# Kernel optimization log

Hardware: AMD Instinct MI355X
Metric: run time of the kernel (lower is better)

The kernel has to match this reference:

```python
import jax, jax.numpy as jnp
import numpy as np

D_MODEL = 1024
D_INNER = 2048
D_STATE = 16
DT_RANK = 64  # ceil(1024/16)
N_LAYERS = 4
SEQ = 4096


def setup_inputs() -> dict:
    key = jax.random.key(0)
    ks = list(jax.random.split(key, 8))
    L, d, di, n, r = N_LAYERS, D_MODEL, D_INNER, D_STATE, DT_RANK
    def rn(k, shape, scale):
        return jax.random.normal(k, shape, dtype=jnp.float32) * scale
    A_init = jnp.tile(jnp.log(jnp.arange(1, n + 1, dtype=jnp.float32))[None, None, :], (L, di, 1))
    return {
        'x': jax.random.normal(ks[0], (SEQ, d), dtype=jnp.float32),
        'pos_enc': jax.random.normal(ks[1], (SEQ, d), dtype=jnp.float32),
        'ln_g': jnp.ones((d,), jnp.float32),
        'ln_b': jnp.zeros((d,), jnp.float32),
        'innorm_g': jnp.ones((L, d), jnp.float32),
        'innorm_b': jnp.zeros((L, d), jnp.float32),
        'in_proj_w': rn(ks[2], (L, 2 * di, d), 0.02),
        'in_proj_b': jnp.zeros((L, 2 * di), jnp.float32),
        'conv_w': rn(ks[3], (L, di, 1, 3), 0.1),
        'conv_b': jnp.zeros((L, di), jnp.float32),
        'deltaBC_w': rn(ks[4], (L, r + 2 * n, di), 0.02),
        'dt_proj_w': rn(ks[5], (L, di, r), 0.02),
        'dt_proj_b': jnp.zeros((L, di), jnp.float32),
        'A_log': A_init,
        'Dp': jnp.ones((L, di), jnp.float32),
        'outnorm_g': jnp.ones((L, di), jnp.float32),
        'outnorm_b': jnp.zeros((L, di), jnp.float32),
        'out_proj_w': rn(ks[6], (L, d, di), 0.02),
        'out_proj_b': jnp.zeros((L, d), jnp.float32),
    }


def _ln(x, g, b, eps):
    mu = jnp.mean(x, axis=-1, keepdims=True)
    var = jnp.mean((x - mu) ** 2, axis=-1, keepdims=True)
    return (x - mu) * jax.lax.rsqrt(var + eps) * g + b


def _selective_scan(u, delta, A, B, C, D):
    # u, delta: [b,l,d]; A: [d,n]; B, C: [b,l,n]; D: [d]
    b, l, d = u.shape
    n = A.shape[1]
    def step(h, inputs):
        d_t, B_t, u_t, C_t = inputs          # [b,d],[b,n],[b,d],[b,n]
        dA = jnp.exp(d_t[:, :, None] * A)    # [b,d,n]
        dBu = (d_t * u_t)[:, :, None] * B_t[:, None, :]
        h = dA * h + dBu
        y = jnp.einsum('bdn,bn->bd', h, C_t)
        return h, y
    h0 = jnp.zeros((b, d, n), u.dtype)
    xs = (jnp.swapaxes(delta, 0, 1), jnp.swapaxes(B, 0, 1),
          jnp.swapaxes(u, 0, 1), jnp.swapaxes(C, 0, 1))
    _, ys = jax.lax.scan(step, h0, xs)       # ys: [l,b,d]
    return jnp.swapaxes(ys, 0, 1) + u * D


def _block(x, innorm_g, innorm_b, in_proj_w, in_proj_b, conv_w, conv_b,
           deltaBC_w, dt_proj_w, dt_proj_b, A_log, Dp, outnorm_g, outnorm_b,
           out_proj_w, out_proj_b):
    skip = x
    h = _ln(x, innorm_g, innorm_b, 1e-5)
    xz = h @ in_proj_w.T + in_proj_b
    x1, z1 = jnp.split(xz, 2, axis=-1)       # [b,s,di] each
    # depthwise conv1d, k=3, pad=1
    xc = jnp.swapaxes(x1, 1, 2)              # [b,di,s]
    xc = jax.lax.conv_general_dilated(xc, conv_w, (1,), [(1, 1)],
                                      feature_group_count=xc.shape[1],
                                      dimension_numbers=('NCH', 'OIH', 'NCH'))
    xc = xc + conv_b[None, :, None]
    u = jnp.swapaxes(xc, 1, 2)               # [b,s,di]
    # SSM
    A = -jnp.exp(A_log)
    dbc = u @ deltaBC_w.T                    # [b,s,r+2n]
    delta, B, C = jnp.split(dbc, [DT_RANK, DT_RANK + D_STATE], axis=-1)
    delta = jax.nn.softplus(delta @ dt_proj_w.T + dt_proj_b)
    y = _selective_scan(u, delta, A, B, C, Dp)
    y = _ln(y, outnorm_g, outnorm_b, 1e-5)
    out = y * jax.nn.silu(z1)
    return out @ out_proj_w.T + out_proj_b + skip


def _forward(x, pos_enc, ln_g, ln_b, innorm_g, innorm_b, in_proj_w, in_proj_b,
             conv_w, conv_b, deltaBC_w, dt_proj_w, dt_proj_b, A_log, Dp,
             outnorm_g, outnorm_b, out_proj_w, out_proj_b):
    enc = _ln(x + pos_enc, ln_g, ln_b, 1e-6)[None]  # [1,s,d]
    for i in range(N_LAYERS):
        enc = _block(enc, innorm_g[i], innorm_b[i], in_proj_w[i], in_proj_b[i],
                     conv_w[i], conv_b[i], deltaBC_w[i], dt_proj_w[i],
                     dt_proj_b[i], A_log[i], Dp[i], outnorm_g[i], outnorm_b[i],
                     out_proj_w[i], out_proj_b[i])
    return enc[0]


def reference(x, pos_enc, ln_g, ln_b, innorm_g, innorm_b, in_proj_w, in_proj_b,
              conv_w, conv_b, deltaBC_w, dt_proj_w, dt_proj_b, A_log, Dp,
              outnorm_g, outnorm_b, out_proj_w, out_proj_b):
    return _forward(x, pos_enc, ln_g, ln_b, innorm_g, innorm_b, in_proj_w,
                    in_proj_b, conv_w, conv_b, deltaBC_w, dt_proj_w, dt_proj_b,
                    A_log, Dp, outnorm_g, outnorm_b, out_proj_w, out_proj_b)
```

## Files before the change

### kernel.cpp

```cpp
#include <hip/hip_runtime.h>
#include <hip/hip_bf16.h>
#include <stdint.h>


#define SEQ     4096
#define DMODEL  1024
#define DINNER  2048
#define NSTATE  16
#define DTRANK  64
#define NLAYERS 4
#define LC      64
#define NC      64

typedef __attribute__((ext_vector_type(8))) short short8v;
typedef __attribute__((ext_vector_type(4))) float f32x4;
typedef __hip_bfloat16 bf16;

__device__ __forceinline__ float b2f(unsigned short x) {
    unsigned int u = ((unsigned int)x) << 16;
    return __builtin_bit_cast(float, u);
}

__device__ __forceinline__ void gld16(const void* gsrc, void* ldst) {
    __builtin_amdgcn_global_load_lds(
        (const __attribute__((address_space(1))) void*)gsrc,
        (__attribute__((address_space(3))) void*)ldst, 16, 0, 0);
}

__device__ __forceinline__ float block_sum(float v, float* red, int nwaves) {
    #pragma unroll
    for (int o = 32; o > 0; o >>= 1) v += __shfl_down(v, o, 64);
    int lane = threadIdx.x & 63, w = threadIdx.x >> 6;
    __syncthreads();
    if (lane == 0) red[w] = v;
    __syncthreads();
    float s = red[0];
    for (int i = 1; i < nwaves; i++) s += red[i];
    return s;
}

template<int WIDTH, typename OutT>
__global__ void ln_kernel(const float* __restrict__ X, const float* __restrict__ X2,
                          const float* __restrict__ g, const float* __restrict__ bta,
                          OutT* __restrict__ out, float eps) {
    constexpr int E = WIDTH / 256;
    __shared__ float red[4];
    int s = blockIdx.x, tid = threadIdx.x;
    size_t base = (size_t)s * WIDTH;
    float v[E]; float sum = 0.f;
    #pragma unroll
    for (int i = 0; i < E; i++) {
        int c = tid + i * 256;
        float t = X[base + c];
        if (X2) t += X2[base + c];
        v[i] = t; sum += t;
    }
    float mu = block_sum(sum, red, 4) * (1.f / WIDTH);
    float sq = 0.f;
    #pragma unroll
    for (int i = 0; i < E; i++) { float d = v[i] - mu; sq += d * d; }
    float var = block_sum(sq, red, 4) * (1.f / WIDTH);
    float rstd = rsqrtf(var + eps);
    #pragma unroll
    for (int i = 0; i < E; i++) {
        int c = tid + i * 256;
        float r = (v[i] - mu) * rstd * g[c] + bta[c];
        out[base + c] = (OutT)r;
    }
}

__global__ void outnorm_silu_kernel(const float* __restrict__ y, const bf16* __restrict__ xz,
                                    const float* __restrict__ g, const float* __restrict__ bta,
                                    bf16* __restrict__ p_bf, float eps) {
    constexpr int WIDTH = DINNER, E = WIDTH / 256;
    __shared__ float red[4];
    int s = blockIdx.x, tid = threadIdx.x;
    size_t base = (size_t)s * WIDTH;
    const unsigned short* xzu = (const unsigned short*)xz;
    float v[E]; float sum = 0.f;
    #pragma unroll
    for (int i = 0; i < E; i++) { int c = tid + i * 256; v[i] = y[base + c]; sum += v[i]; }
    float mu = block_sum(sum, red, 4) * (1.f / WIDTH);
    float sq = 0.f;
    #pragma unroll
    for (int i = 0; i < E; i++) { float d = v[i] - mu; sq += d * d; }
    float var = block_sum(sq, red, 4) * (1.f / WIDTH);
    float rstd = rsqrtf(var + eps);
    #pragma unroll
    for (int i = 0; i < E; i++) {
        int c = tid + i * 256;
        float ln = (v[i] - mu) * rstd * g[c] + bta[c];
        float z = b2f(xzu[(size_t)s * (2 * DINNER) + DINNER + c]);
        float sig = 1.f / (1.f + __expf(-z));
        p_bf[base + c] = __float2bfloat16(ln * (z * sig));
    }
}

__global__ void conv_kernel(const bf16* __restrict__ xz, const float* __restrict__ cw,
                            const float* __restrict__ cb, bf16* __restrict__ u_bf) {
    int t = blockIdx.x * 256 + threadIdx.x;
    int s = t >> 9, c = (t & 511) * 4;
    size_t row = (size_t)s * (2 * DINNER);
    const unsigned short* xp = (const unsigned short*)xz;
    ushort4 z4 = {0, 0, 0, 0};
    ushort4 v0 = *(const ushort4*)(xp + row + c);
    ushort4 vm = (s > 0)       ? *(const ushort4*)(xp + row - 2 * DINNER + c) : z4;
    ushort4 vp = (s < SEQ - 1) ? *(const ushort4*)(xp + row + 2 * DINNER + c) : z4;
    unsigned short o[4];
    float x0[4] = {b2f(v0.x), b2f(v0.y), b2f(v0.z), b2f(v0.w)};
    float xm[4] = {b2f(vm.x), b2f(vm.y), b2f(vm.z), b2f(vm.w)};
    float xp4[4] = {b2f(vp.x), b2f(vp.y), b2f(vp.z), b2f(vp.w)};
    #pragma unroll
    for (int i = 0; i < 4; i++) {
        int ch = c + i;
        float u = cw[ch * 3 + 0] * xm[i] + cw[ch * 3 + 1] * x0[i]
                + cw[ch * 3 + 2] * xp4[i] + cb[ch];
        o[i] = __builtin_bit_cast(unsigned short, __float2bfloat16(u));
    }
    *(ushort4*)((unsigned short*)u_bf + (size_t)s * DINNER + c) = {o[0], o[1], o[2], o[3]};
}

#define CN0 (2 * DINNER * DMODEL)
#define CN1 (DMODEL * DINNER)
#define CN2 (96 * DINNER)
#define CN3 (DINNER * DTRANK)
__global__ void cvt_all_kernel(const float* __restrict__ w0, const float* __restrict__ w1,
                               const float* __restrict__ w2, const float* __restrict__ w3,
                               bf16* __restrict__ o0, bf16* __restrict__ o1,
                               bf16* __restrict__ o2, bf16* __restrict__ o3) {
    size_t i = (size_t)(blockIdx.x * 256 + threadIdx.x) * 4;
    const float* src; bf16* dst;
    if (i < CN0)                   { src = w0; dst = o0; }
    else if (i < CN0 + CN1)        { src = w1; dst = o1; i -= CN0; }
    else if (i < CN0 + CN1 + CN2)  { src = w2; dst = o2; i -= CN0 + CN1; }
    else                           { src = w3; dst = o3; i -= CN0 + CN1 + CN2; }
    float4 v = *(const float4*)(src + i);
    __hip_bfloat162 t0, t1;
    t0.x = __float2bfloat16(v.x); t0.y = __float2bfloat16(v.y);
    t1.x = __float2bfloat16(v.z); t1.y = __float2bfloat16(v.w);
    __hip_bfloat162* o = (__hip_bfloat162*)(dst + i);
    o[0] = t0; o[1] = t1;
}

template<int MODE>
__global__ __launch_bounds__(256, 2)
void mfma_gemm(const bf16* __restrict__ A, int lda,
               const bf16* __restrict__ W, int ldw,
               const float* __restrict__ bias,
               float* __restrict__ C, int ldc,
               const float* __restrict__ res,
               bf16* __restrict__ Cbf,
               int M, int N, int K) {
    __shared__ __attribute__((aligned(16))) short sA[128][32];
    __shared__ __attribute__((aligned(16))) short sB[128][32];
    int tid = threadIdx.x;
    int lane = tid & 63, w = tid >> 6;
    int wm = w >> 1, wn = w & 1;
    int m0 = blockIdx.x * 128, n0 = blockIdx.y * 128;
    int r16 = lane & 15, quad = lane >> 4;
    int ldrow = (lane >> 2);
    int c8 = (lane & 3) * 8;

    if (MODE == 1) {
        int kz = blockIdx.z;
        A += (size_t)kz * K;
        W += (size_t)kz * K;
        C += (size_t)kz * M * 96;
    }

    f32x4 acc[4][4] = {};

    for (int k0 = 0; k0 < K; k0 += 32) {
        __syncthreads();
        #pragma unroll
        for (int j = 0; j < 2; j++) {
            int row = j * 64 + w * 16 + ldrow;
            gld16(A + (size_t)(m0 + row) * lda + k0 + c8,
                  (char*)&sA[0][0] + j * 4096 + w * 1024);
            int nr = n0 + row; if (nr > N - 1) nr = N - 1;
            gld16(W + (size_t)nr * ldw + k0 + c8,
                  (char*)&sB[0][0] + j * 4096 + w * 1024);
        }
        __syncthreads();
        short8v aF[4], bF[4];
        #pragma unroll
        for (int mi = 0; mi < 4; mi++)
            aF[mi] = *(const short8v*)&sA[wm * 64 + mi * 16 + r16][quad * 8];
        #pragma unroll
        for (int ni = 0; ni < 4; ni++)
            bF[ni] = *(const short8v*)&sB[wn * 64 + ni * 16 + r16][quad * 8];
        #pragma unroll
        for (int mi = 0; mi < 4; mi++)
            #pragma unroll
            for (int ni = 0; ni < 4; ni++)
                acc[mi][ni] = __builtin_amdgcn_mfma_f32_16x16x32_bf16(
                    aF[mi], bF[ni], acc[mi][ni], 0, 0, 0);
    }

    #pragma unroll
    for (int mi = 0; mi < 4; mi++) {
        #pragma unroll
        for (int ni = 0; ni < 4; ni++) {
            f32x4 a = acc[mi][ni];
            int col = n0 + wn * 64 + ni * 16 + r16;
            int rbase = m0 + wm * 64 + mi * 16 + quad * 4;
            #pragma unroll
            for (int r = 0; r < 4; r++) {
                int row = rbase + r;
                float v = a[r];
                if (MODE == 0 || MODE == 2 || MODE == 3) v += bias[col];
                if (MODE == 2) v = (v > 20.f) ? v : log1pf(__expf(v));
                if (MODE == 3) v += res[(size_t)row * ldc + col];
                if (MODE == 1) {
                    if (col < 96) C[(size_t)row * 96 + col] = v;
                } else if (MODE == 0) {
                    Cbf[(size_t)row * ldc + col] = __float2bfloat16(v);
                } else {
                    C[(size_t)row * ldc + col] = v;
                }
            }
        }
    }
}

__global__ void reduce_dbc_kernel(const float* __restrict__ p, float* __restrict__ dbc,
                                  bf16* __restrict__ dbc_bf) {
    int i = blockIdx.x * 256 + threadIdx.x;
    const int SP = SEQ * 96;
    float v = p[i] + p[i + SP] + p[i + 2 * SP] + p[i + 3 * SP];
    dbc[i] = v;
    int row = i / 96, c = i - row * 96;
    if (c < DTRANK) dbc_bf[(size_t)row * DTRANK + c] = __float2bfloat16(v);
}

__device__ __forceinline__ bool a_is_neg_integers(const float* a) {
    bool fast = true;
    #pragma unroll
    for (int n = 0; n < NSTATE; n++)
        fast = fast && (__builtin_fabsf(a[n] + (float)(n + 1)) < 1e-3f * (n + 1));
    return fast;
}

__global__ void scan1_kernel(const float* __restrict__ delta, const bf16* __restrict__ u,
                             const float* __restrict__ dbc, const float* __restrict__ A_log,
                             float* __restrict__ h_end, float* __restrict__ dsum) {
    __shared__ __attribute__((aligned(16))) float sB[LC][NSTATE];
    int k = blockIdx.x, d = blockIdx.y * 256 + threadIdx.x;
    int s0 = k * LC, tid = threadIdx.x;
    #pragma unroll
    for (int i = 0; i < 4; i++) {
        int idx = tid + i * 256;
        int r = idx >> 4, n = idx & 15;
        sB[r][n] = dbc[(size_t)(s0 + r) * 96 + DTRANK + n];
    }
    float a[NSTATE];
    #pragma unroll
    for (int n = 0; n < NSTATE; n++) a[n] = -__expf(A_log[(size_t)d * NSTATE + n]);
    bool fast = a_is_neg_integers(a);
    __syncthreads();
    const unsigned short* uu16 = (const unsigned short*)u;
    float h[NSTATE] = {}; float ds = 0.f;
    if (fast) {
        #pragma unroll 2
        for (int r = 0; r < LC; r++) {
            float dl = delta[(size_t)(s0 + r) * DINNER + d];
            float du = dl * b2f(uu16[(size_t)(s0 + r) * DINNER + d]);
            ds += dl;
            float g = __expf(-dl);
            float Bv[NSTATE];
            #pragma unroll
            for (int q = 0; q < 4; q++) *(float4*)&Bv[q * 4] = *(const float4*)&sB[r][q * 4];
            float fac = 1.f;
            #pragma unroll
            for (int n = 0; n < NSTATE; n++) {
                fac *= g;
                h[n] = fac * h[n] + du * Bv[n];
            }
        }
    } else {
        #pragma unroll 2
        for (int r = 0; r < LC; r++) {
            float dl = delta[(size_t)(s0 + r) * DINNER + d];
            float du = dl * b2f(uu16[(size_t)(s0 + r) * DINNER + d]);
            ds += dl;
            float Bv[NSTATE];
            #pragma unroll
            for (int q = 0; q < 4; q++) *(float4*)&Bv[q * 4] = *(const float4*)&sB[r][q * 4];
            #pragma unroll
            for (int n = 0; n < NSTATE; n++)
                h[n] = __expf(dl * a[n]) * h[n] + du * Bv[n];
        }
    }
    #pragma unroll
    for (int n = 0; n < NSTATE; n++)
        h_end[((size_t)k * NSTATE + n) * DINNER + d] = h[n];
    dsum[(size_t)k * DINNER + d] = ds;
}

__global__ void scan2_kernel(const float* __restrict__ A_log, const float* __restrict__ dsum,
                             const float* __restrict__ h_end, float* __restrict__ hinit) {
    int id = blockIdx.x * 256 + threadIdx.x;
    int d = id & (DINNER - 1), n = id >> 11;
    float a = -__expf(A_log[(size_t)d * NSTATE + n]);
    float h = 0.f;
    for (int k = 0; k < NC; k++) {
        size_t off = ((size_t)k * NSTATE + n) * DINNER + d;
        hinit[off] = h;
        h = __expf(a * dsum[(size_t)k * DINNER + d]) * h + h_end[off];
    }
}

__global__ void scan3_kernel(float* __restrict__ delta_y, const bf16* __restrict__ u,
                             const float* __restrict__ dbc, const float* __restrict__ A_log,
                             const float* __restrict__ Dp, const float* __restrict__ hinit) {
    __shared__ __attribute__((aligned(16))) float sB[LC][NSTATE];
    __shared__ __attribute__((aligned(16))) float sC[LC][NSTATE];
    int k = blockIdx.x, d = blockIdx.y * 256 + threadIdx.x;
    int s0 = k * LC, tid = threadIdx.x;
    #pragma unroll
    for (int i = 0; i < 8; i++) {
        int idx = tid + i * 256;
        int r = idx >> 5, c = idx & 31;
        float v = dbc[(size_t)(s0 + r) * 96 + DTRANK + c];
        if (c < 16) sB[r][c] = v; else sC[r][c - 16] = v;
    }
    float a[NSTATE];
    #pragma unroll
    for (int n = 0; n < NSTATE; n++) a[n] = -__expf(A_log[(size_t)d * NSTATE + n]);
    bool fast = a_is_neg_integers(a);
    float h[NSTATE];
    #pragma unroll
    for (int n = 0; n < NSTATE; n++)
        h[n] = hinit[((size_t)k * NSTATE + n) * DINNER + d];
    float dpv = Dp[d];
    __syncthreads();
    const unsigned short* uu16 = (const unsigned short*)u;
    if (fast) {
        #pragma unroll 2
        for (int r = 0; r < LC; r++) {
            float dl = delta_y[(size_t)(s0 + r) * DINNER + d];
            float uu = b2f(uu16[(size_t)(s0 + r) * DINNER + d]);
            float du = dl * uu;
            float g = __expf(-dl);
            float Bv[NSTATE], Cv[NSTATE];
            #pragma unroll
            for (int q = 0; q < 4; q++) {
                *(float4*)&Bv[q * 4] = *(const float4*)&sB[r][q * 4];
                *(float4*)&Cv[q * 4] = *(const float4*)&sC[r][q * 4];
            }
            float y = uu * dpv;
            float fac = 1.f;
            #pragma unroll
            for (int n = 0; n < NSTATE; n++) {
                fac *= g;
                h[n] = fac * h[n] + du * Bv[n];
                y += h[n] * Cv[n];
            }
            delta_y[(size_t)(s0 + r) * DINNER + d] = y;
        }
    } else {
        #pragma unroll 2
        for (int r = 0; r < LC; r++) {
            float dl = delta_y[(size_t)(s0 + r) * DINNER + d];
            float uu = b2f(uu16[(size_t)(s0 + r) * DINNER + d]);
            float du = dl * uu;
            float Bv[NSTATE], Cv[NSTATE];
            #pragma unroll
            for (int q = 0; q < 4; q++) {
                *(float4*)&Bv[q * 4] = *(const float4*)&sB[r][q * 4];
                *(float4*)&Cv[q * 4] = *(const float4*)&sC[r][q * 4];
            }
            float y = uu * dpv;
            #pragma unroll
            for (int n = 0; n < NSTATE; n++) {
                h[n] = __expf(dl * a[n]) * h[n] + du * Bv[n];
                y += h[n] * Cv[n];
            }
            delta_y[(size_t)(s0 + r) * DINNER + d] = y;
        }
    }
}

extern "C" void kernel_launch(void* const* d_in, const int* in_sizes, int n_in,
                              void* d_out, int out_size, void* d_ws, size_t ws_size,
                              hipStream_t stream) {
    const float* x         = (const float*)d_in[0];
    const float* pos       = (const float*)d_in[1];
    const float* ln_g      = (const float*)d_in[2];
    const float* ln_b      = (const float*)d_in[3];
    const float* innorm_g  = (const float*)d_in[4];
    const float* innorm_b  = (const float*)d_in[5];
    const float* in_proj_w = (const float*)d_in[6];
    const float* in_proj_b = (const float*)d_in[7];
    const float* conv_w    = (const float*)d_in[8];
    const float* conv_b    = (const float*)d_in[9];
    const float* deltaBC_w = (const float*)d_in[10];
    const float* dt_proj_w = (const float*)d_in[11];
    const float* dt_proj_b = (const float*)d_in[12];
    const float* A_log     = (const float*)d_in[13];
    const float* Dp        = (const float*)d_in[14];
    const float* outnorm_g = (const float*)d_in[15];
    const float* outnorm_b = (const float*)d_in[16];
    const float* out_proj_w= (const float*)d_in[17];
    const float* out_proj_b= (const float*)d_in[18];

    float* enc = (float*)d_out;
    char* ws = (char*)d_ws;
    const size_t MB = 1024 * 1024;
    bf16*  h_bf   = (bf16*) (ws + 0);
    bf16*  p_bf   = (bf16*) (ws + 0);
    bf16*  xz_bf  = (bf16*) (ws + 16 * MB);
    float* dlt    = (float*)(ws + 48 * MB);
    float* dbcp   = (float*)(ws + 48 * MB);
    bf16*  u_bf   = (bf16*) (ws + 80 * MB);
    float* dbc    = (float*)(ws + 96 * MB);
    bf16*  dbc_bf = (bf16*) (ws + 98 * MB);
    float* h_end  = (float*)(ws + 99 * MB);
    float* hinit  = (float*)(ws + 107 * MB);
    float* dsum   = (float*)(ws + 115 * MB);
    bf16*  w_in   = (bf16*) (ws + 116 * MB);
    bf16*  w_dbc  = (bf16*) (ws + 124 * MB);
    bf16*  w_dt   = (bf16*) (ws + 125 * MB);
    bf16*  w_out  = (bf16*) (ws + 126 * MB);

    ln_kernel<DMODEL, float><<<SEQ, 256, 0, stream>>>(x, pos, ln_g, ln_b, enc, 1e-6f);

    for (int L = 0; L < NLAYERS; L++) {
        const float* Al = A_log + (size_t)L * DINNER * NSTATE;
        cvt_all_kernel<<<(CN0 + CN1 + CN2 + CN3) / 1024, 256, 0, stream>>>(
            in_proj_w + (size_t)L * CN0, out_proj_w + (size_t)L * CN1,
            deltaBC_w + (size_t)L * CN2, dt_proj_w + (size_t)L * CN3,
            w_in, w_out, w_dbc, w_dt);

        ln_kernel<DMODEL, bf16><<<SEQ, 256, 0, stream>>>(enc, nullptr, innorm_g + L * DMODEL,
                                                         innorm_b + L * DMODEL, h_bf, 1e-5f);
        mfma_gemm<0><<<dim3(32, 32), 256, 0, stream>>>(
            h_bf, DMODEL, w_in, DMODEL, in_proj_b + (size_t)L * 2 * DINNER,
            nullptr, 2 * DINNER, nullptr, xz_bf, SEQ, 2 * DINNER, DMODEL);
        conv_kernel<<<(SEQ * 512) / 256, 256, 0, stream>>>(
            xz_bf, conv_w + (size_t)L * DINNER * 3, conv_b + L * DINNER, u_bf);
        mfma_gemm<1><<<dim3(32, 1, 4), 256, 0, stream>>>(
            u_bf, DINNER, w_dbc, DINNER, nullptr,
            dbcp, 96, nullptr, nullptr, SEQ, 96, 512);
        reduce_dbc_kernel<<<(SEQ * 96) / 256, 256, 0, stream>>>(dbcp, dbc, dbc_bf);
        mfma_gemm<2><<<dim3(32, 16), 256, 0, stream>>>(
            dbc_bf, DTRANK, w_dt, DTRANK, dt_proj_b + L * DINNER,
            dlt, DINNER, nullptr, nullptr, SEQ, DINNER, DTRANK);
        scan1_kernel<<<dim3(NC, DINNER / 256), 256, 0, stream>>>(dlt, u_bf, dbc, Al, h_end, dsum);
        scan2_kernel<<<(DINNER * NSTATE) / 256, 256, 0, stream>>>(Al, dsum, h_end, hinit);
        scan3_kernel<<<dim3(NC, DINNER / 256), 256, 0, stream>>>(dlt, u_bf, dbc, Al,
                                                                 Dp + L * DINNER, hinit);
        outnorm_silu_kernel<<<SEQ, 256, 0, stream>>>(dlt, xz_bf, outnorm_g + L * DINNER,
                                                     outnorm_b + L * DINNER, p_bf, 1e-5f);
        mfma_gemm<3><<<dim3(32, 8), 256, 0, stream>>>(
            p_bf, DINNER, w_out, DINNER, out_proj_b + L * DMODEL,
            enc, DMODEL, enc, nullptr, SEQ, DMODEL, DINNER);
    }
}
```

Baseline: 1.116 ms.

## Fuse dt_proj GEMM and softplus into both selective-scan passes

Removes the separate dt_proj GEMM that wrote the fp32 delta tensor. Each scan block now computes its own 64x256 tile of delta with MFMA from dbc_bf and w_dt staged in LDS, applies bias and softplus, and feeds the scan through a shared-memory buffer. The aim is to stop writing and re-reading the SEQ×DINNER delta array twice. In exchange the small GEMM is computed twice (in pass 1 and pass 3), there are extra LDS traffic and barriers per 16-row group, and register pressure goes up.

```diff
diff --git a/kernel.cpp b/kernel.cpp
--- a/kernel.cpp
+++ b/kernel.cpp
@@ -208,8 +208,7 @@
             for (int r = 0; r < 4; r++) {
                 int row = rbase + r;
                 float v = a[r];
-                if (MODE == 0 || MODE == 2 || MODE == 3) v += bias[col];
-                if (MODE == 2) v = (v > 20.f) ? v : log1pf(__expf(v));
+                if (MODE == 0 || MODE == 3) v += bias[col];
                 if (MODE == 3) v += res[(size_t)row * ldc + col];
                 if (MODE == 1) {
                     if (col < 96) C[(size_t)row * 96 + col] = v;
@@ -241,60 +240,178 @@
     return fast;
 }
 
-__global__ void scan1_kernel(const float* __restrict__ delta, const bf16* __restrict__ u,
-                             const float* __restrict__ dbc, const float* __restrict__ A_log,
-                             float* __restrict__ h_end, float* __restrict__ dsum) {
+template<int PASS3>
+__global__ __launch_bounds__(256, 2)
+void scanf_kernel(const bf16* __restrict__ dbc_bf, const bf16* __restrict__ wdt,
+                  const float* __restrict__ dtb, const bf16* __restrict__ u,
+                  const float* __restrict__ dbc, const float* __restrict__ A_log,
+                  const float* __restrict__ Dp, const float* __restrict__ hio,
+                  float* __restrict__ out1, float* __restrict__ out2) {
+    __shared__ __attribute__((aligned(16))) short sDbc[64][64];
+    __shared__ __attribute__((aligned(16))) short sWdt[256][64];
+    __shared__ __attribute__((aligned(16))) float sDelta[16][256];
     __shared__ __attribute__((aligned(16))) float sB[LC][NSTATE];
-    int k = blockIdx.x, d = blockIdx.y * 256 + threadIdx.x;
+    __shared__ __attribute__((aligned(16))) float sC[PASS3 ? LC : 1][NSTATE];
+    int k = blockIdx.x, d0 = blockIdx.y * 256;
     int s0 = k * LC, tid = threadIdx.x;
-    #pragma unroll
-    for (int i = 0; i < 4; i++) {
-        int idx = tid + i * 256;
-        int r = idx >> 4, n = idx & 15;
-        sB[r][n] = dbc[(size_t)(s0 + r) * 96 + DTRANK + n];
+    int lane = tid & 63, w = tid >> 6;
+    int r16 = lane & 15, quad = lane >> 4;
+    int d = d0 + tid;
+
+    #pragma unroll
+    for (int i = 0; i < 2; i++) {
+        int idx = i * 256 + tid;
+        int r = idx >> 3, c = (idx & 7) ^ (r & 7);
+        gld16(dbc_bf + (size_t)(s0 + r) * DTRANK + c * 8,
+              (char*)&sDbc[0][0] + i * 4096 + w * 1024);
+    }
+    #pragma unroll
+    for (int i = 0; i < 8; i++) {
+        int idx = i * 256 + tid;
+        int r = idx >> 3, c = (idx & 7) ^ (r & 7);
+        gld16(wdt + (size_t)(d0 + r) * DTRANK + c * 8,
+              (char*)&sWdt[0][0] + i * 4096 + w * 1024);
+    }
+    if (PASS3) {
+        #pragma unroll
+        for (int i = 0; i < 8; i++) {
+            int idx = tid + i * 256;
+            int r = idx >> 5, c = idx & 31;
+            float v = dbc[(size_t)(s0 + r) * 96 + DTRANK + c];
+            if (c < 16) sB[r][c] = v; else sC[r][c - 16] = v;
+        }
+    } else {
+        #pragma unroll
+        for (int i = 0; i < 4; i++) {
+            int idx = tid + i * 256;
+            int r = idx >> 4, n = idx & 15;
+            sB[r][n] = dbc[(size_t)(s0 + r) * 96 + DTRANK + n];
+        }
     }
     float a[NSTATE];
     #pragma unroll
     for (int n = 0; n < NSTATE; n++) a[n] = -__expf(A_log[(size_t)d * NSTATE + n]);
     bool fast = a_is_neg_integers(a);
     __syncthreads();
+
+    short8v aF[4][2], bF[4][2];
+    #pragma unroll
+    for (int m = 0; m < 4; m++)
+        #pragma unroll
+        for (int kk = 0; kk < 2; kk++)
+            aF[m][kk] = *(const short8v*)&sDbc[m * 16 + r16][((kk * 4 + quad) ^ (r16 & 7)) * 8];
+    #pragma unroll
+    for (int n = 0; n < 4; n++)
+        #pragma unroll
+        for (int kk = 0; kk < 2; kk++)
+            bF[n][kk] = *(const short8v*)&sWdt[w * 64 + n * 16 + r16][((kk * 4 + quad) ^ (r16 & 7)) * 8];
+    f32x4 acc[4][4] = {};
+    #pragma unroll
+    for (int m = 0; m < 4; m++)
+        #pragma unroll
+        for (int n = 0; n < 4; n++) {
+            acc[m][n] = __builtin_amdgcn_mfma_f32_16x16x32_bf16(aF[m][0], bF[n][0], acc[m][n], 0, 0, 0);
+            acc[m][n] = __builtin_amdgcn_mfma_f32_16x16x32_bf16(aF[m][1], bF[n][1], acc[m][n], 0, 0, 0);
+        }
+    #pragma unroll
+    for (int n = 0; n < 4; n++) {
+        float bs = dtb[d0 + w * 64 + n * 16 + r16];
+        #pragma unroll
+        for (int m = 0; m < 4; m++)
+            #pragma unroll
+            for (int rg = 0; rg < 4; rg++) {
+                float v = acc[m][n][rg] + bs;
+                acc[m][n][rg] = (v > 20.f) ? v : log1pf(__expf(v));
+            }
+    }
+
+    float h[NSTATE];
+    #pragma unroll
+    for (int n = 0; n < NSTATE; n++)
+        h[n] = PASS3 ? hio[((size_t)k * NSTATE + n) * DINNER + d] : 0.f;
+    float ds = 0.f;
+    float dpv = PASS3 ? Dp[d] : 0.f;
     const unsigned short* uu16 = (const unsigned short*)u;
-    float h[NSTATE] = {}; float ds = 0.f;
-    if (fast) {
-        #pragma unroll 2
-        for (int r = 0; r < LC; r++) {
-            float dl = delta[(size_t)(s0 + r) * DINNER + d];
-            float du = dl * b2f(uu16[(size_t)(s0 + r) * DINNER + d]);
-            ds += dl;
-            float g = __expf(-dl);
-            float Bv[NSTATE];
+
+    #pragma unroll
+    for (int g = 0; g < 4; g++) {
+        if (g) __syncthreads();
+        #pragma unroll
+        for (int n = 0; n < 4; n++)
             #pragma unroll
-            for (int q = 0; q < 4; q++) *(float4*)&Bv[q * 4] = *(const float4*)&sB[r][q * 4];
-            float fac = 1.f;
-            #pragma unroll
-            for (int n = 0; n < NSTATE; n++) {
-                fac *= g;
-                h[n] = fac * h[n] + du * Bv[n];
+            for (int rg = 0; rg < 4; rg++)
+                sDelta[quad * 4 + rg][w * 64 + n * 16 + r16] = acc[g][n][rg];
+        __syncthreads();
+        if (fast) {
+            #pragma unroll 4
+            for (int rr = 0; rr < 16; rr++) {
+                int r = g * 16 + rr;
+                float dl = sDelta[rr][tid];
+                float uu = b2f(uu16[(size_t)(s0 + r) * DINNER + d]);
+                float du = dl * uu;
+                float gx = __expf(-dl);
+                float Bv[NSTATE];
+                #pragma unroll
+                for (int q = 0; q < 4; q++) *(float4*)&Bv[q * 4] = *(const float4*)&sB[r][q * 4];
+                if (PASS3) {
+                    float Cv[NSTATE];
+                    #pragma unroll
+                    for (int q = 0; q < 4; q++) *(float4*)&Cv[q * 4] = *(const float4*)&sC[r][q * 4];
+                    float y = uu * dpv;
+                    float fac = 1.f;
+                    #pragma unroll
+                    for (int n = 0; n < NSTATE; n++) {
+                        fac *= gx;
+                        h[n] = fac * h[n] + du * Bv[n];
+                        y += h[n] * Cv[n];
+                    }
+                    out1[(size_t)(s0 + r) * DINNER + d] = y;
+                } else {
+                    ds += dl;
+                    float fac = 1.f;
+                    #pragma unroll
+                    for (int n = 0; n < NSTATE; n++) {
+                        fac *= gx;
+                        h[n] = fac * h[n] + du * Bv[n];
+                    }
+                }
+            }
+        } else {
+            #pragma unroll 2
+            for (int rr = 0; rr < 16; rr++) {
+                int r = g * 16 + rr;
+                float dl = sDelta[rr][tid];
+                float uu = b2f(uu16[(size_t)(s0 + r) * DINNER + d]);
+                float du = dl * uu;
+                float Bv[NSTATE];
+                #pragma unroll
+                for (int q = 0; q < 4; q++) *(float4*)&Bv[q * 4] = *(const float4*)&sB[r][q * 4];
+                if (PASS3) {
+                    float Cv[NSTATE];
+                    #pragma unroll
+                    for (int q = 0; q < 4; q++) *(float4*)&Cv[q * 4] = *(const float4*)&sC[r][q * 4];
+                    float y = uu * dpv;
+                    #pragma unroll
+                    for (int n = 0; n < NSTATE; n++) {
+                        h[n] = __expf(dl * a[n]) * h[n] + du * Bv[n];
+                        y += h[n] * Cv[n];
+                    }
+                    out1[(size_t)(s0 + r) * DINNER + d] = y;
+                } else {
+                    ds += dl;
+                    #pragma unroll
+                    for (int n = 0; n < NSTATE; n++)
+                        h[n] = __expf(dl * a[n]) * h[n] + du * Bv[n];
+                }
             }
         }
-    } else {
-        #pragma unroll 2
-        for (int r = 0; r < LC; r++) {
-            float dl = delta[(size_t)(s0 + r) * DINNER + d];
-            float du = dl * b2f(uu16[(size_t)(s0 + r) * DINNER + d]);
-            ds += dl;
-            float Bv[NSTATE];
-            #pragma unroll
-            for (int q = 0; q < 4; q++) *(float4*)&Bv[q * 4] = *(const float4*)&sB[r][q * 4];
-            #pragma unroll
-            for (int n = 0; n < NSTATE; n++)
-                h[n] = __expf(dl * a[n]) * h[n] + du * Bv[n];
-        }
-    }
-    #pragma unroll
-    for (int n = 0; n < NSTATE; n++)
-        h_end[((size_t)k * NSTATE + n) * DINNER + d] = h[n];
-    dsum[(size_t)k * DINNER + d] = ds;
+    }
+    if (!PASS3) {
+        #pragma unroll
+        for (int n = 0; n < NSTATE; n++)
+            out1[((size_t)k * NSTATE + n) * DINNER + d] = h[n];
+        out2[(size_t)k * DINNER + d] = ds;
+    }
 }
 
 __global__ void scan2_kernel(const float* __restrict__ A_log, const float* __restrict__ dsum,
@@ -307,77 +424,6 @@
         size_t off = ((size_t)k * NSTATE + n) * DINNER + d;
         hinit[off] = h;
         h = __expf(a * dsum[(size_t)k * DINNER + d]) * h + h_end[off];
-    }
-}
-
-__global__ void scan3_kernel(float* __restrict__ delta_y, const bf16* __restrict__ u,
-                             const float* __restrict__ dbc, const float* __restrict__ A_log,
-                             const float* __restrict__ Dp, const float* __restrict__ hinit) {
-    __shared__ __attribute__((aligned(16))) float sB[LC][NSTATE];
-    __shared__ __attribute__((aligned(16))) float sC[LC][NSTATE];
-    int k = blockIdx.x, d = blockIdx.y * 256 + threadIdx.x;
-    int s0 = k * LC, tid = threadIdx.x;
-    #pragma unroll
-    for (int i = 0; i < 8; i++) {
-        int idx = tid + i * 256;
-        int r = idx >> 5, c = idx & 31;
-        float v = dbc[(size_t)(s0 + r) * 96 + DTRANK + c];
-        if (c < 16) sB[r][c] = v; else sC[r][c - 16] = v;
-    }
-    float a[NSTATE];
-    #pragma unroll
-    for (int n = 0; n < NSTATE; n++) a[n] = -__expf(A_log[(size_t)d * NSTATE + n]);
-    bool fast = a_is_neg_integers(a);
-    float h[NSTATE];
-    #pragma unroll
-    for (int n = 0; n < NSTATE; n++)
-        h[n] = hinit[((size_t)k * NSTATE + n) * DINNER + d];
-    float dpv = Dp[d];
-    __syncthreads();
-    const unsigned short* uu16 = (const unsigned short*)u;
-    if (fast) {
-        #pragma unroll 2
-        for (int r = 0; r < LC; r++) {
-            float dl = delta_y[(size_t)(s0 + r) * DINNER + d];
-            float uu = b2f(uu16[(size_t)(s0 + r) * DINNER + d]);
-            float du = dl * uu;
-            float g = __expf(-dl);
-            float Bv[NSTATE], Cv[NSTATE];
-            #pragma unroll
-            for (int q = 0; q < 4; q++) {
-                *(float4*)&Bv[q * 4] = *(const float4*)&sB[r][q * 4];
-                *(float4*)&Cv[q * 4] = *(const float4*)&sC[r][q * 4];
-            }
-            float y = uu * dpv;
-            float fac = 1.f;
-            #pragma unroll
-            for (int n = 0; n < NSTATE; n++) {
-                fac *= g;
-                h[n] = fac * h[n] + du * Bv[n];
-                y += h[n] * Cv[n];
-            }
-            delta_y[(size_t)(s0 + r) * DINNER + d] = y;
-        }
-    } else {
-        #pragma unroll 2
-        for (int r = 0; r < LC; r++) {
-            float dl = delta_y[(size_t)(s0 + r) * DINNER + d];
-            float uu = b2f(uu16[(size_t)(s0 + r) * DINNER + d]);
-            float du = dl * uu;
-            float Bv[NSTATE], Cv[NSTATE];
-            #pragma unroll
-            for (int q = 0; q < 4; q++) {
-                *(float4*)&Bv[q * 4] = *(const float4*)&sB[r][q * 4];
-                *(float4*)&Cv[q * 4] = *(const float4*)&sC[r][q * 4];
-            }
-            float y = uu * dpv;
-            #pragma unroll
-            for (int n = 0; n < NSTATE; n++) {
-                h[n] = __expf(dl * a[n]) * h[n] + du * Bv[n];
-                y += h[n] * Cv[n];
-            }
-            delta_y[(size_t)(s0 + r) * DINNER + d] = y;
-        }
     }
 }
 
@@ -443,13 +489,13 @@
             u_bf, DINNER, w_dbc, DINNER, nullptr,
             dbcp, 96, nullptr, nullptr, SEQ, 96, 512);
         reduce_dbc_kernel<<<(SEQ * 96) / 256, 256, 0, stream>>>(dbcp, dbc, dbc_bf);
-        mfma_gemm<2><<<dim3(32, 16), 256, 0, stream>>>(
-            dbc_bf, DTRANK, w_dt, DTRANK, dt_proj_b + L * DINNER,
-            dlt, DINNER, nullptr, nullptr, SEQ, DINNER, DTRANK);
-        scan1_kernel<<<dim3(NC, DINNER / 256), 256, 0, stream>>>(dlt, u_bf, dbc, Al, h_end, dsum);
+        scanf_kernel<0><<<dim3(NC, DINNER / 256), 256, 0, stream>>>(
+            dbc_bf, w_dt, dt_proj_b + (size_t)L * DINNER, u_bf, dbc, Al,
+            nullptr, nullptr, h_end, dsum);
         scan2_kernel<<<(DINNER * NSTATE) / 256, 256, 0, stream>>>(Al, dsum, h_end, hinit);
-        scan3_kernel<<<dim3(NC, DINNER / 256), 256, 0, stream>>>(dlt, u_bf, dbc, Al,
-                                                                 Dp + L * DINNER, hinit);
+        scanf_kernel<1><<<dim3(NC, DINNER / 256), 256, 0, stream>>>(
+            dbc_bf, w_dt, dt_proj_b + (size_t)L * DINNER, u_bf, dbc, Al,
+            Dp + L * DINNER, hinit, dlt, nullptr);
         outnorm_silu_kernel<<<SEQ, 256, 0, stream>>>(dlt, xz_bf, outnorm_g + L * DINNER,
                                                      outnorm_b + L * DINNER, p_bf, 1e-5f);
         mfma_gemm<3><<<dim3(32, 8), 256, 0, stream>>>(
```

Measured after the change: 1.212 ms. +8.6%, slower.
